# Kernel optimization log

Measured on AMD Instinct MI355X. Metric: run time of the kernel, lower is better.

Reference implementation:

```python
import jax, jax.numpy as jnp
import numpy as np

N = 8192
D_MODEL = 1024
KEY_DIM = 64
OUT_DIM = 1024
N_HEADS = 1
SCALE = N_HEADS ** (-0.5)  # = 1.0
NEG_INF = -1e10  # matches tf -10000000000.0


def setup_inputs() -> dict:
    key = jax.random.key(0)
    ks = jax.random.split(key, 3)
    x = jax.random.normal(ks[0], (N, D_MODEL), dtype=jnp.float32)
    w_qkv = jax.random.normal(ks[1], (D_MODEL, 3 * KEY_DIM), dtype=jnp.float32) * (D_MODEL ** -0.5)
    b_qkv = jnp.zeros((3 * KEY_DIM,), dtype=jnp.float32)
    w_out = jax.random.normal(ks[2], (KEY_DIM, OUT_DIM), dtype=jnp.float32) * (KEY_DIM ** -0.5)
    b_out = jnp.zeros((OUT_DIM,), dtype=jnp.float32)
    return {"x": x, "w_qkv": w_qkv, "b_qkv": b_qkv, "w_out": w_out, "b_out": b_out, "causal": 1}


def reference(x, w_qkv, b_qkv, w_out, b_out, causal):
    n = x.shape[-2]
    qkv = x @ w_qkv + b_qkv                      # [n, 3*key_dim]
    q, k, v = jnp.split(qkv, 3, axis=-1)         # each [n, key_dim]
    sim = jnp.einsum('id,jd->ij', q, k) * SCALE  # [n, n]
    if causal:
        mask = jnp.tril(jnp.ones((n, n), dtype=bool))
        sim = jnp.where(mask, sim, NEG_INF)
    attn = jax.nn.softmax(sim, axis=-1)          # [n, n]
    out = jnp.einsum('ij,jd->id', attn, v)       # [n, key_dim]
    return out @ w_out + b_out                   # [n, out_dim]
```

## Files before the change

### kernel.cpp

```cpp
#include <hip/hip_runtime.h>
#include <hip/hip_bf16.h>
#include <math.h>

#define N_TOK 8192
#define DM 1024
#define KD 64
#define ODIM 1024
#define LOG2E 1.4426950408889634f

typedef unsigned short ushort_t;
typedef __attribute__((ext_vector_type(8))) short short8;
typedef __attribute__((ext_vector_type(4))) float f32x4;

#define MFMA16(a, b, c) __builtin_amdgcn_mfma_f32_16x16x32_bf16((a), (b), (c), 0, 0, 0)

__device__ __forceinline__ float ex2(float x) {
#if __has_builtin(__builtin_amdgcn_exp2f)
    return __builtin_amdgcn_exp2f(x);
#else
    return exp2f(x);
#endif
}
__device__ __forceinline__ ushort_t rne(float x) {
    unsigned u = __float_as_uint(x);
    u += 0x7fffu + ((u >> 16) & 1u);
    return (ushort_t)(u >> 16);
}
__device__ __forceinline__ float ubf(ushort_t h) {
    return __uint_as_float(((unsigned)h) << 16);
}
__device__ __forceinline__ void split2(float x, ushort_t& hi, ushort_t& lo) {
    hi = rne(x);
    lo = rne(x - ubf(hi));
}
__device__ __forceinline__ unsigned bfpack(float a, float b) {
    unsigned ua = __float_as_uint(a); ua += 0x7fffu + ((ua >> 16) & 1u);
    unsigned ub = __float_as_uint(b); ub += 0x7fffu + ((ub >> 16) & 1u);
    return (ua >> 16) | (ub & 0xffff0000u);
}
__device__ __forceinline__ void gld_lds16(const void* g, void* l) {
    __builtin_amdgcn_global_load_lds(
        (const __attribute__((address_space(1))) unsigned int*)g,
        (__attribute__((address_space(3))) unsigned int*)l, 16, 0, 0);
}

__global__ __launch_bounds__(256) void prep_kernel(
    const float* __restrict__ wq, const float* __restrict__ wo,
    const float* __restrict__ x,
    ushort_t* __restrict__ wT_hi, ushort_t* __restrict__ wT_lo,
    ushort_t* __restrict__ woT_hi, ushort_t* __restrict__ woT_lo,
    ushort_t* __restrict__ x_hi, ushort_t* __restrict__ x_lo)
{
    const int idx = blockIdx.x * 256 + threadIdx.x;
    if (idx < 192 * 1024) {
        const int c = idx >> 10, k = idx & 1023;
        ushort_t h, l; split2(wq[k * 192 + c], h, l);
        wT_hi[idx] = h; wT_lo[idx] = l;
    } else if (idx < 256 * 1024) {
        const int j = idx - 192 * 1024;
        const int c = j >> 6, k = j & 63;
        ushort_t h, l; split2(wo[k * ODIM + c], h, l);
        woT_hi[j] = h; woT_lo[j] = l;
    } else {
        const size_t j = (size_t)(idx - 256 * 1024) * 8;
        const float4 xa = *(const float4*)&x[j];
        const float4 xb = *(const float4*)&x[j + 4];
        const float xe[8] = {xa.x, xa.y, xa.z, xa.w, xb.x, xb.y, xb.z, xb.w};
        union { short8 v; ushort_t u[8]; } hh, ll;
#pragma unroll
        for (int e = 0; e < 8; ++e) { split2(xe[e], hh.u[e], ll.u[e]); }
        *(short8*)&x_hi[j] = hh.v;
        *(short8*)&x_lo[j] = ll.v;
    }
}

__global__ __launch_bounds__(256) void qkv_kernel(
    const ushort_t* __restrict__ x_hi, const ushort_t* __restrict__ x_lo,
    const ushort_t* __restrict__ wT_hi, const ushort_t* __restrict__ wT_lo,
    const float* __restrict__ b,
    ushort_t* __restrict__ q_hi, ushort_t* __restrict__ q_lo,
    ushort_t* __restrict__ k_hi, ushort_t* __restrict__ k_lo,
    ushort_t* __restrict__ vT)
{
    __shared__ ushort_t S[2][20480];

    const int tid = threadIdx.x;
    const int wv = tid >> 6, lane = tid & 63, g = lane >> 4, i = lane & 15;
    const int bb = (int)blockIdx.x;
    const int R0 = (bb >> 1) * 64, h = bb & 1;
    const int rh = wv >> 1, cq = wv & 1;
    const int sub = lane >> 3, s = lane & 7;
    const f32x4 zero4 = {0.f, 0.f, 0.f, 0.f};

    auto stage = [&](int buf, int t) {
        const int kb = t * 64;
#pragma unroll
        for (int j = 0; j < 10; ++j) {
            const int c = wv + 4 * j;
            ushort_t* dst = &S[buf][c << 9];
            const ushort_t* src;
            if (j < 4) {
                const int r = ((c & 7) << 3) + sub;
                src = (j < 2 ? x_hi : x_lo) +
                      (size_t)(R0 + r) * DM + kb + ((s ^ (r & 7)) << 3);
            } else if (j < 7) {
                const int wc = ((c - 16) << 3) + sub;
                src = wT_hi + (size_t)(h * 96 + wc) * DM + kb + ((s ^ (wc & 7)) << 3);
            } else {
                const int wc = ((c - 28) << 3) + sub;
                src = wT_lo + (size_t)(h * 96 + wc) * DM + kb + ((s ^ (wc & 7)) << 3);
            }
            gld_lds16(src, dst);
        }
    };

    f32x4 acc[2][3] = {{zero4, zero4, zero4}, {zero4, zero4, zero4}};

    stage(0, 0);

    for (int t = 0; t < 16; ++t) {
        const int cur = t & 1;
        if (t + 1 < 16) {
            stage(cur ^ 1, t + 1);
            asm volatile("s_waitcnt vmcnt(10)" ::: "memory");
        } else {
            asm volatile("s_waitcnt vmcnt(0)" ::: "memory");
        }
        __builtin_amdgcn_s_barrier();

        const ushort_t* Sb = S[cur];
        short8 ah[2][2], al[2][2], bh[3][2], bl[3][2];
#pragma unroll
        for (int a = 0; a < 2; ++a) {
            const int r = (rh << 5) + (a << 4) + i;
#pragma unroll
            for (int kf = 0; kf < 2; ++kf) {
                const int off = (r << 6) + (((g + (kf << 2)) ^ (r & 7)) << 3);
                ah[a][kf] = *(const short8*)&Sb[off];
                al[a][kf] = *(const short8*)&Sb[4096 + off];
            }
        }
#pragma unroll
        for (int ct = 0; ct < 3; ++ct) {
            const int wc = cq * 48 + (ct << 4) + i;
#pragma unroll
            for (int kf = 0; kf < 2; ++kf) {
                const int off = (wc << 6) + (((g + (kf << 2)) ^ (wc & 7)) << 3);
                bh[ct][kf] = *(const short8*)&Sb[8192 + off];
                bl[ct][kf] = *(const short8*)&Sb[14336 + off];
            }
        }
#pragma unroll
        for (int a = 0; a < 2; ++a)
#pragma unroll
            for (int ct = 0; ct < 3; ++ct) {
                f32x4 v = acc[a][ct];
                v = MFMA16(ah[a][0], bh[ct][0], v);
                v = MFMA16(ah[a][1], bh[ct][1], v);
                v = MFMA16(ah[a][0], bl[ct][0], v);
                v = MFMA16(ah[a][1], bl[ct][1], v);
                v = MFMA16(al[a][0], bh[ct][0], v);
                v = MFMA16(al[a][1], bh[ct][1], v);
                acc[a][ct] = v;
            }
        asm volatile("s_waitcnt lgkmcnt(0)" ::: "memory");
        __builtin_amdgcn_s_barrier();
    }

#pragma unroll
    for (int ct = 0; ct < 3; ++ct) {
        const int ctid = h * 6 + cq * 3 + ct;
        const int col = (ctid << 4) + i;
        const float bias = b[col];
#pragma unroll
        for (int a = 0; a < 2; ++a) {
            const int row0 = R0 + (rh << 5) + (a << 4) + (g << 2);
            if (ctid < 4) {
#pragma unroll
                for (int reg = 0; reg < 4; ++reg) {
                    ushort_t hh, ll; split2((acc[a][ct][reg] + bias) * LOG2E, hh, ll);
                    q_hi[(row0 + reg) * KD + col] = hh;
                    q_lo[(row0 + reg) * KD + col] = ll;
                }
            } else if (ctid < 8) {
                const int c2 = col - 64;
#pragma unroll
                for (int reg = 0; reg < 4; ++reg) {
                    ushort_t hh, ll; split2(acc[a][ct][reg] + bias, hh, ll);
                    k_hi[(row0 + reg) * KD + c2] = hh;
                    k_lo[(row0 + reg) * KD + c2] = ll;
                }
            } else {
                union { ushort_t u[4]; uint2 v; } pk;
#pragma unroll
                for (int reg = 0; reg < 4; ++reg) pk.u[reg] = rne(acc[a][ct][reg] + bias);
                *(uint2*)&vT[(size_t)(col - 128) * N_TOK + row0] = pk.v;
            }
        }
    }
}

__global__ __launch_bounds__(256) void attn_kernel(
    const ushort_t* __restrict__ q_hi, const ushort_t* __restrict__ q_lo,
    const ushort_t* __restrict__ k_hi, const ushort_t* __restrict__ k_lo,
    const ushort_t* __restrict__ vT,
    float* __restrict__ Opart, float* __restrict__ MLpart,
    const int* __restrict__ causal_p, const int LC, const int ACT)
{
    __shared__ ushort_t Kls[2][2][4096];

    const int tid = threadIdx.x;
    const int wv = tid >> 6, lane = tid & 63, g = lane >> 4, i = lane & 15;
    const int causal = *causal_p;
    const f32x4 zero4 = {0.f, 0.f, 0.f, 0.f};
    const int ibase = ((i >> 2) << 3) + (i & 3);

    const int bb = (int)blockIdx.x;
    int gb, chunk;
    if (bb < ACT) {
        const int Q = 1 << (LC - 1);
        int a = (int)((sqrtf((float)bb / (float)Q + 0.25f) - 0.5f));
        while (a > 0 && a * (a + 1) * Q > bb) --a;
        while ((a + 1) * (a + 2) * Q <= bb) ++a;
        const int r = bb - a * (a + 1) * Q;
        const int b2 = r / (a + 1);
        chunk = r - b2 * (a + 1);
        gb = (a << LC) + b2;
    } else {
        const int j = bb - ACT;
        gb = j & 127; chunk = j >> 7;
        if (chunk <= (gb >> LC)) return;
    }
    const int nkt = causal ? gb + 1 : (N_TOK / 64);
    const int t0 = chunk << LC;
    if (t0 >= nkt) return;
    const int tmax = t0 + (1 << LC);
    const int t1 = tmax < nkt ? tmax : nkt;
    const int R0w = (gb << 6) + (wv << 4);

    const short8 qh0 = *(const short8*)&q_hi[(R0w + i) * KD + g * 8];
    const short8 qh1 = *(const short8*)&q_hi[(R0w + i) * KD + 32 + g * 8];
    const short8 ql0 = *(const short8*)&q_lo[(R0w + i) * KD + g * 8];
    const short8 ql1 = *(const short8*)&q_lo[(R0w + i) * KD + 32 + g * 8];

    const int srow = lane >> 3;
    const int sslot = lane & 7;
    auto stageK = [&](int nb, int t) {
        const int kb2 = t << 6;
#pragma unroll
        for (int h = 0; h < 2; ++h) {
            const int ch = wv + (h << 2);
            const int row = (ch << 3) + srow;
            const int sw = ((row & 3) << 1) | ((row >> 3) & 1);
            const size_t src = (size_t)(kb2 + row) * KD + ((sslot ^ sw) << 3);
            gld_lds16(&k_hi[src], &Kls[nb][0][ch << 9]);
            gld_lds16(&k_lo[src], &Kls[nb][1][ch << 9]);
        }
    };

    f32x4 o4[4] = {zero4, zero4, zero4, zero4};
    float runm = -1e30f, runl = 0.f;

    stageK(0, t0);

    for (int t = t0; t < t1; ++t) {
        const int cur = (t - t0) & 1;
        const int kb = t << 6;
        const bool more = (t + 1 < t1);

        short8 va0[4], va1[4];
#pragma unroll
        for (int ct2 = 0; ct2 < 4; ++ct2) {
            const size_t vrow = (size_t)(ct2 * 16 + i) * N_TOK + kb;
            va0[ct2] = *(const short8*)&vT[vrow + g * 8];
            va1[ct2] = *(const short8*)&vT[vrow + 32 + g * 8];
        }
        if (more) {
            stageK(cur ^ 1, t + 1);
            asm volatile("s_waitcnt vmcnt(12)" ::: "memory");
        } else {
            asm volatile("s_waitcnt vmcnt(8)" ::: "memory");
        }
        __builtin_amdgcn_s_barrier();

        f32x4 s4[4];
#pragma unroll
        for (int ct = 0; ct < 4; ++ct) {
            const int r = ((ct & 1) << 2) + ((ct >> 1) << 5) + ibase;
            const int sw = ((r & 3) << 1) | ((r >> 3) & 1);
            const ushort_t* khp = &Kls[cur][0][r << 6];
            const ushort_t* klp = &Kls[cur][1][r << 6];
            const short8 kh0 = *(const short8*)&khp[(g ^ sw) << 3];
            const short8 kh1 = *(const short8*)&khp[((g + 4) ^ sw) << 3];
            const short8 kl0 = *(const short8*)&klp[(g ^ sw) << 3];
            const short8 kl1 = *(const short8*)&klp[((g + 4) ^ sw) << 3];
            f32x4 a = MFMA16(kh0, qh0, zero4);
            a = MFMA16(kh1, qh1, a);
            a = MFMA16(kh0, ql0, a);
            a = MFMA16(kh1, ql1, a);
            a = MFMA16(kl0, qh0, a);
            a = MFMA16(kl1, qh1, a);
            s4[ct] = a;
        }
        asm volatile("s_waitcnt lgkmcnt(0)" ::: "memory");
        __builtin_amdgcn_s_barrier();

        if (causal && (kb + 64 > R0w)) {
#pragma unroll
            for (int ct = 0; ct < 4; ++ct) {
                const int kba = kb + ((ct & 1) << 2) + ((ct >> 1) << 5);
#pragma unroll
                for (int reg = 0; reg < 4; ++reg) {
                    const int key = kba + (g << 3) + reg;
                    s4[ct][reg] = (key <= R0w + i) ? s4[ct][reg] : -1e30f;
                }
            }
        }
        float mx = -1e30f;
#pragma unroll
        for (int ct = 0; ct < 4; ++ct)
#pragma unroll
            for (int reg = 0; reg < 4; ++reg) mx = fmaxf(mx, s4[ct][reg]);
        mx = fmaxf(mx, __shfl_xor(mx, 16));
        mx = fmaxf(mx, __shfl_xor(mx, 32));
        const bool defer = __all(mx - runm <= 8.0f);
        const float nm = defer ? runm : fmaxf(runm, mx);
        const float al = defer ? 1.0f : ex2(runm - nm);
        runm = nm;
        float rs = 0.f;
#pragma unroll
        for (int ct = 0; ct < 4; ++ct)
#pragma unroll
            for (int reg = 0; reg < 4; ++reg) {
                const float p = ex2(s4[ct][reg] - nm);
                s4[ct][reg] = p;
                rs += p;
            }
        rs += __shfl_xor(rs, 16);
        rs += __shfl_xor(rs, 32);
        runl = runl * al + rs;
        if (!defer) {
#pragma unroll
            for (int ct2 = 0; ct2 < 4; ++ct2)
#pragma unroll
                for (int reg = 0; reg < 4; ++reg) o4[ct2][reg] *= al;
        }
        short8 pb0, pb1;
        {
            union { unsigned w[4]; short8 v; } u;
            u.w[0] = bfpack(s4[0][0], s4[0][1]); u.w[1] = bfpack(s4[0][2], s4[0][3]);
            u.w[2] = bfpack(s4[1][0], s4[1][1]); u.w[3] = bfpack(s4[1][2], s4[1][3]);
            pb0 = u.v;
            u.w[0] = bfpack(s4[2][0], s4[2][1]); u.w[1] = bfpack(s4[2][2], s4[2][3]);
            u.w[2] = bfpack(s4[3][0], s4[3][1]); u.w[3] = bfpack(s4[3][2], s4[3][3]);
            pb1 = u.v;
        }
        if (more) asm volatile("s_waitcnt vmcnt(4)" ::: "memory");
        else      asm volatile("s_waitcnt vmcnt(0)" ::: "memory");
#pragma unroll
        for (int ct2 = 0; ct2 < 4; ++ct2) {
            o4[ct2] = MFMA16(va0[ct2], pb0, o4[ct2]);
            o4[ct2] = MFMA16(va1[ct2], pb1, o4[ct2]);
        }
    }

    const int pidx = ((gb << (7 - LC)) + chunk) * 4 + wv;
#pragma unroll
    for (int ct2 = 0; ct2 < 4; ++ct2)
#pragma unroll
        for (int reg = 0; reg < 4; ++reg) {
            const int d = ct2 * 16 + 4 * g + reg;
            Opart[((size_t)pidx * 16 + i) * 64 + d] = o4[ct2][reg];
        }
    if (lane < 16) {
        MLpart[pidx * 32 + lane] = runm;
        MLpart[pidx * 32 + 16 + lane] = runl;
    }
}

__global__ __launch_bounds__(256) void merge_kernel(
    const float* __restrict__ Opart, const float* __restrict__ MLpart,
    ushort_t* __restrict__ aoh, ushort_t* __restrict__ aol,
    const int* __restrict__ causal_p, const int LC)
{
    const int idx = blockIdx.x * 256 + threadIdx.x;
    const int d = idx & 63, row = idx >> 6;
    const int r = row & 15, qtile = row >> 4, gb = row >> 6;
    const int causal = *causal_p;
    const int nkt = causal ? gb + 1 : (N_TOK / 64);
    const int nch = (nkt + (1 << LC) - 1) >> LC;
    const int pb = ((gb << (7 - LC)) << 2) + (qtile & 3);
    float m[16], l[16];
#pragma unroll
    for (int c = 0; c < 16; ++c) {
        if (c < nch) {
            m[c] = MLpart[(pb + 4 * c) * 32 + r];
            l[c] = MLpart[(pb + 4 * c) * 32 + 16 + r];
        } else { m[c] = -1e30f; l[c] = 0.f; }
    }
    float M = m[0];
#pragma unroll
    for (int c = 1; c < 16; ++c) M = fmaxf(M, m[c]);
    float den = 0.f, O = 0.f;
#pragma unroll
    for (int c = 0; c < 16; ++c) {
        const float e = ex2(m[c] - M);
        den += l[c] * e;
        if (c < nch)
            O += Opart[((size_t)(pb + 4 * c) * 16 + r) * 64 + d] * e;
    }
    ushort_t h, lo2; split2(O / den, h, lo2);
    aoh[row * 64 + d] = h;
    aol[row * 64 + d] = lo2;
}

__global__ __launch_bounds__(256) void proj_kernel(
    const ushort_t* __restrict__ aoh, const ushort_t* __restrict__ aol,
    const ushort_t* __restrict__ woT_hi, const ushort_t* __restrict__ woT_lo,
    const float* __restrict__ bo, float* __restrict__ out)
{
    const int tid = threadIdx.x;
    const int wv = tid >> 6, lane = tid & 63, g = lane >> 4, i = lane & 15;
    const int bb = (int)blockIdx.x;
    const int qtile = bb >> 2, qa = bb & 3;
    const int R0 = qtile << 4;
    const f32x4 zero4 = {0.f, 0.f, 0.f, 0.f};
    const short8 ah0 = *(const short8*)&aoh[(R0 + i) * 64 + g * 8];
    const short8 ah1 = *(const short8*)&aoh[(R0 + i) * 64 + 32 + g * 8];
    const short8 al0 = *(const short8*)&aol[(R0 + i) * 64 + g * 8];
    const short8 al1 = *(const short8*)&aol[(R0 + i) * 64 + 32 + g * 8];
#pragma unroll
    for (int cc = 0; cc < 4; ++cc) {
        const int col = (qa << 8) + ((wv << 2) + cc) * 16 + i;
        const short8 bh0 = *(const short8*)&woT_hi[col * KD + g * 8];
        const short8 bh1 = *(const short8*)&woT_hi[col * KD + 32 + g * 8];
        const short8 bl0 = *(const short8*)&woT_lo[col * KD + g * 8];
        const short8 bl1 = *(const short8*)&woT_lo[col * KD + 32 + g * 8];
        f32x4 acc = MFMA16(ah0, bh0, zero4);
        acc = MFMA16(ah1, bh1, acc);
        acc = MFMA16(ah0, bl0, acc);
        acc = MFMA16(ah1, bl1, acc);
        acc = MFMA16(al0, bh0, acc);
        acc = MFMA16(al1, bh1, acc);
        const float bias = bo[col];
#pragma unroll
        for (int reg = 0; reg < 4; ++reg)
            out[(size_t)(R0 + 4 * g + reg) * ODIM + col] = acc[reg] + bias;
    }
}

extern "C" void kernel_launch(void* const* d_in, const int* in_sizes, int n_in,
                              void* d_out, int out_size, void* d_ws, size_t ws_size,
                              hipStream_t stream) {
    const float* x     = (const float*)d_in[0];
    const float* w_qkv = (const float*)d_in[1];
    const float* b_qkv = (const float*)d_in[2];
    const float* w_out = (const float*)d_in[3];
    const float* b_out = (const float*)d_in[4];
    const int* causal  = (const int*)d_in[5];
    float* out         = (float*)d_out;

    const int LC  = (ws_size >= ((size_t)39 << 20)) ? 3 : 4;
    const int NCH = 128 >> LC;
    const int NA  = 128 >> LC;
    const int ACT = (1 << LC) * NA * (NA + 1) / 2;
    const size_t opart_bytes = (size_t)128 * NCH * 4 * 16 * 64 * 4;

    char* ws = (char*)d_ws;
    ushort_t* wT_hi  = (ushort_t*)(ws);
    ushort_t* wT_lo  = (ushort_t*)(ws + 393216);
    ushort_t* woT_hi = (ushort_t*)(ws + 786432);
    ushort_t* woT_lo = (ushort_t*)(ws + 917504);
    ushort_t* q_hi   = (ushort_t*)(ws + (1u << 20));
    ushort_t* q_lo   = (ushort_t*)(ws + (2u << 20));
    ushort_t* k_hi   = (ushort_t*)(ws + (3u << 20));
    ushort_t* k_lo   = (ushort_t*)(ws + (4u << 20));
    ushort_t* vT     = (ushort_t*)(ws + (5u << 20));
    ushort_t* x_hi   = (ushort_t*)(ws + (6u << 20));
    ushort_t* x_lo   = (ushort_t*)(ws + (22u << 20));
    float*    Opart  = (float*)(ws + (6u << 20));
    float*    MLpart = (float*)(ws + (6u << 20) + opart_bytes);
    ushort_t* aoh    = (ushort_t*)(ws + (1u << 20));
    ushort_t* aol    = (ushort_t*)(ws + (2u << 20));

    prep_kernel<<<5120, 256, 0, stream>>>(w_qkv, w_out, x, wT_hi, wT_lo,
                                          woT_hi, woT_lo, x_hi, x_lo);
    qkv_kernel<<<256, 256, 0, stream>>>(x_hi, x_lo, wT_hi, wT_lo, b_qkv,
                                        q_hi, q_lo, k_hi, k_lo, vT);
    attn_kernel<<<ACT + NCH * 128, 256, 0, stream>>>(q_hi, q_lo, k_hi, k_lo, vT,
                                                     Opart, MLpart, causal, LC, ACT);
    merge_kernel<<<2048, 256, 0, stream>>>(Opart, MLpart, aoh, aol, causal, LC);
    proj_kernel<<<2048, 256, 0, stream>>>(aoh, aol, woT_hi, woT_lo, b_out, out);
}
```

Before: 194.1 us.

## Double attention block to 8 waves over 128 query rows sharing K tiles

Attention blocks now use 512 threads, with each of 8 waves handling 16 query rows, so one staged K tile in LDS serves 128 queries instead of 64. This halves global K traffic and LDS staging per query. Each wave now issues one K load pair instead of two, and the block grid is remapped over 128-row query groups. Waves whose rows lie entirely before the causal diagonal skip compute but still join the barriers. The cost is idle waves on diagonal tiles, and larger blocks may lower occupancy or scheduling flexibility.

Result: slower. 199.5 us (+2.8%).

```diff
diff --git a/kernel.cpp b/kernel.cpp
--- a/kernel.cpp
+++ b/kernel.cpp
@@ -200,7 +200,7 @@
     }
 }
 
-__global__ __launch_bounds__(256) void attn_kernel(
+__global__ __launch_bounds__(512) void attn_kernel(
     const ushort_t* __restrict__ q_hi, const ushort_t* __restrict__ q_lo,
     const ushort_t* __restrict__ k_hi, const ushort_t* __restrict__ k_lo,
     const ushort_t* __restrict__ vT,
@@ -216,27 +216,31 @@
     const int ibase = ((i >> 2) << 3) + (i & 3);
 
     const int bb = (int)blockIdx.x;
-    int gb, chunk;
+    const int G = 1 << (LC - 1);
+    int gb2, chunk;
     if (bb < ACT) {
-        const int Q = 1 << (LC - 1);
-        int a = (int)((sqrtf((float)bb / (float)Q + 0.25f) - 0.5f));
-        while (a > 0 && a * (a + 1) * Q > bb) --a;
-        while ((a + 1) * (a + 2) * Q <= bb) ++a;
-        const int r = bb - a * (a + 1) * Q;
+        int a = (int)(sqrtf((float)(2 * bb) / (float)G + 0.25f) - 0.5f);
+        while (a > 0 && G * a * (a + 1) / 2 > bb) --a;
+        while (G * (a + 1) * (a + 2) / 2 <= bb) ++a;
+        const int r = bb - G * a * (a + 1) / 2;
         const int b2 = r / (a + 1);
         chunk = r - b2 * (a + 1);
-        gb = (a << LC) + b2;
+        gb2 = G * a + b2;
     } else {
         const int j = bb - ACT;
-        gb = j & 127; chunk = j >> 7;
-        if (chunk <= (gb >> LC)) return;
-    }
-    const int nkt = causal ? gb + 1 : (N_TOK / 64);
+        gb2 = j & 63; chunk = j >> 6;
+        if (chunk <= (gb2 >> (LC - 1))) return;
+    }
+    const int nktB = causal ? 2 * gb2 + 2 : (N_TOK / 64);
     const int t0 = chunk << LC;
-    if (t0 >= nkt) return;
+    if (t0 >= nktB) return;
     const int tmax = t0 + (1 << LC);
-    const int t1 = tmax < nkt ? tmax : nkt;
-    const int R0w = (gb << 6) + (wv << 4);
+    const int t1 = tmax < nktB ? tmax : nktB;
+
+    const int qt = gb2 * 8 + wv;
+    const int R0w = qt << 4;
+    const int myNkt = causal ? (R0w >> 6) + 1 : (N_TOK / 64);
+    const int t1w = t1 < myNkt ? t1 : myNkt;
 
     const short8 qh0 = *(const short8*)&q_hi[(R0w + i) * KD + g * 8];
     const short8 qh1 = *(const short8*)&q_hi[(R0w + i) * KD + 32 + g * 8];
@@ -247,15 +251,11 @@
     const int sslot = lane & 7;
     auto stageK = [&](int nb, int t) {
         const int kb2 = t << 6;
-#pragma unroll
-        for (int h = 0; h < 2; ++h) {
-            const int ch = wv + (h << 2);
-            const int row = (ch << 3) + srow;
-            const int sw = ((row & 3) << 1) | ((row >> 3) & 1);
-            const size_t src = (size_t)(kb2 + row) * KD + ((sslot ^ sw) << 3);
-            gld_lds16(&k_hi[src], &Kls[nb][0][ch << 9]);
-            gld_lds16(&k_lo[src], &Kls[nb][1][ch << 9]);
-        }
+        const int row = (wv << 3) + srow;
+        const int sw = ((row & 3) << 1) | ((row >> 3) & 1);
+        const size_t src = (size_t)(kb2 + row) * KD + ((sslot ^ sw) << 3);
+        gld_lds16(&k_hi[src], &Kls[nb][0][wv << 9]);
+        gld_lds16(&k_lo[src], &Kls[nb][1][wv << 9]);
     };
 
     f32x4 o4[4] = {zero4, zero4, zero4, zero4};
@@ -267,104 +267,114 @@
         const int cur = (t - t0) & 1;
         const int kb = t << 6;
         const bool more = (t + 1 < t1);
+        const bool act = (t < t1w);
 
         short8 va0[4], va1[4];
-#pragma unroll
-        for (int ct2 = 0; ct2 < 4; ++ct2) {
-            const size_t vrow = (size_t)(ct2 * 16 + i) * N_TOK + kb;
-            va0[ct2] = *(const short8*)&vT[vrow + g * 8];
-            va1[ct2] = *(const short8*)&vT[vrow + 32 + g * 8];
+        if (act) {
+#pragma unroll
+            for (int ct2 = 0; ct2 < 4; ++ct2) {
+                const size_t vrow = (size_t)(ct2 * 16 + i) * N_TOK + kb;
+                va0[ct2] = *(const short8*)&vT[vrow + g * 8];
+                va1[ct2] = *(const short8*)&vT[vrow + 32 + g * 8];
+            }
         }
         if (more) {
             stageK(cur ^ 1, t + 1);
-            asm volatile("s_waitcnt vmcnt(12)" ::: "memory");
+            if (act) asm volatile("s_waitcnt vmcnt(10)" ::: "memory");
+            else     asm volatile("s_waitcnt vmcnt(2)" ::: "memory");
         } else {
-            asm volatile("s_waitcnt vmcnt(8)" ::: "memory");
+            if (act) asm volatile("s_waitcnt vmcnt(8)" ::: "memory");
+            else     asm volatile("s_waitcnt vmcnt(0)" ::: "memory");
         }
         __builtin_amdgcn_s_barrier();
 
-        f32x4 s4[4];
-#pragma unroll
-        for (int ct = 0; ct < 4; ++ct) {
-            const int r = ((ct & 1) << 2) + ((ct >> 1) << 5) + ibase;
-            const int sw = ((r & 3) << 1) | ((r >> 3) & 1);
-            const ushort_t* khp = &Kls[cur][0][r << 6];
-            const ushort_t* klp = &Kls[cur][1][r << 6];
-            const short8 kh0 = *(const short8*)&khp[(g ^ sw) << 3];
-            const short8 kh1 = *(const short8*)&khp[((g + 4) ^ sw) << 3];
-            const short8 kl0 = *(const short8*)&klp[(g ^ sw) << 3];
-            const short8 kl1 = *(const short8*)&klp[((g + 4) ^ sw) << 3];
-            f32x4 a = MFMA16(kh0, qh0, zero4);
-            a = MFMA16(kh1, qh1, a);
-            a = MFMA16(kh0, ql0, a);
-            a = MFMA16(kh1, ql1, a);
-            a = MFMA16(kl0, qh0, a);
-            a = MFMA16(kl1, qh1, a);
-            s4[ct] = a;
-        }
-        asm volatile("s_waitcnt lgkmcnt(0)" ::: "memory");
-        __builtin_amdgcn_s_barrier();
-
-        if (causal && (kb + 64 > R0w)) {
+        if (act) {
+            f32x4 s4[4];
 #pragma unroll
             for (int ct = 0; ct < 4; ++ct) {
-                const int kba = kb + ((ct & 1) << 2) + ((ct >> 1) << 5);
+                const int r = ((ct & 1) << 2) + ((ct >> 1) << 5) + ibase;
+                const int sw = ((r & 3) << 1) | ((r >> 3) & 1);
+                const ushort_t* khp = &Kls[cur][0][r << 6];
+                const ushort_t* klp = &Kls[cur][1][r << 6];
+                const short8 kh0 = *(const short8*)&khp[(g ^ sw) << 3];
+                const short8 kh1 = *(const short8*)&khp[((g + 4) ^ sw) << 3];
+                const short8 kl0 = *(const short8*)&klp[(g ^ sw) << 3];
+                const short8 kl1 = *(const short8*)&klp[((g + 4) ^ sw) << 3];
+                f32x4 a = MFMA16(kh0, qh0, zero4);
+                a = MFMA16(kh1, qh1, a);
+                a = MFMA16(kh0, ql0, a);
+                a = MFMA16(kh1, ql1, a);
+                a = MFMA16(kl0, qh0, a);
+                a = MFMA16(kl1, qh1, a);
+                s4[ct] = a;
+            }
+            asm volatile("s_waitcnt lgkmcnt(0)" ::: "memory");
+            __builtin_amdgcn_s_barrier();
+
+            if (causal && (kb + 64 > R0w)) {
+#pragma unroll
+                for (int ct = 0; ct < 4; ++ct) {
+                    const int kba = kb + ((ct & 1) << 2) + ((ct >> 1) << 5);
+#pragma unroll
+                    for (int reg = 0; reg < 4; ++reg) {
+                        const int key = kba + (g << 3) + reg;
+                        s4[ct][reg] = (key <= R0w + i) ? s4[ct][reg] : -1e30f;
+                    }
+                }
+            }
+            float mx = -1e30f;
+#pragma unroll
+            for (int ct = 0; ct < 4; ++ct)
+#pragma unroll
+                for (int reg = 0; reg < 4; ++reg) mx = fmaxf(mx, s4[ct][reg]);
+            mx = fmaxf(mx, __shfl_xor(mx, 16));
+            mx = fmaxf(mx, __shfl_xor(mx, 32));
+            const bool defer = __all(mx - runm <= 8.0f);
+            const float nm = defer ? runm : fmaxf(runm, mx);
+            const float al = defer ? 1.0f : ex2(runm - nm);
+            runm = nm;
+            float rs = 0.f;
+#pragma unroll
+            for (int ct = 0; ct < 4; ++ct)
 #pragma unroll
                 for (int reg = 0; reg < 4; ++reg) {
-                    const int key = kba + (g << 3) + reg;
-                    s4[ct][reg] = (key <= R0w + i) ? s4[ct][reg] : -1e30f;
+                    const float p = ex2(s4[ct][reg] - nm);
+                    s4[ct][reg] = p;
+                    rs += p;
                 }
-            }
-        }
-        float mx = -1e30f;
-#pragma unroll
-        for (int ct = 0; ct < 4; ++ct)
-#pragma unroll
-            for (int reg = 0; reg < 4; ++reg) mx = fmaxf(mx, s4[ct][reg]);
-        mx = fmaxf(mx, __shfl_xor(mx, 16));
-        mx = fmaxf(mx, __shfl_xor(mx, 32));
-        const bool defer = __all(mx - runm <= 8.0f);
-        const float nm = defer ? runm : fmaxf(runm, mx);
-        const float al = defer ? 1.0f : ex2(runm - nm);
-        runm = nm;
-        float rs = 0.f;
-#pragma unroll
-        for (int ct = 0; ct < 4; ++ct)
-#pragma unroll
-            for (int reg = 0; reg < 4; ++reg) {
-                const float p = ex2(s4[ct][reg] - nm);
-                s4[ct][reg] = p;
-                rs += p;
-            }
-        rs += __shfl_xor(rs, 16);
-        rs += __shfl_xor(rs, 32);
-        runl = runl * al + rs;
-        if (!defer) {
-#pragma unroll
-            for (int ct2 = 0; ct2 < 4; ++ct2)
-#pragma unroll
-                for (int reg = 0; reg < 4; ++reg) o4[ct2][reg] *= al;
-        }
-        short8 pb0, pb1;
-        {
-            union { unsigned w[4]; short8 v; } u;
-            u.w[0] = bfpack(s4[0][0], s4[0][1]); u.w[1] = bfpack(s4[0][2], s4[0][3]);
-            u.w[2] = bfpack(s4[1][0], s4[1][1]); u.w[3] = bfpack(s4[1][2], s4[1][3]);
-            pb0 = u.v;
-            u.w[0] = bfpack(s4[2][0], s4[2][1]); u.w[1] = bfpack(s4[2][2], s4[2][3]);
-            u.w[2] = bfpack(s4[3][0], s4[3][1]); u.w[3] = bfpack(s4[3][2], s4[3][3]);
-            pb1 = u.v;
-        }
-        if (more) asm volatile("s_waitcnt vmcnt(4)" ::: "memory");
-        else      asm volatile("s_waitcnt vmcnt(0)" ::: "memory");
-#pragma unroll
-        for (int ct2 = 0; ct2 < 4; ++ct2) {
-            o4[ct2] = MFMA16(va0[ct2], pb0, o4[ct2]);
-            o4[ct2] = MFMA16(va1[ct2], pb1, o4[ct2]);
-        }
-    }
-
-    const int pidx = ((gb << (7 - LC)) + chunk) * 4 + wv;
+            rs += __shfl_xor(rs, 16);
+            rs += __shfl_xor(rs, 32);
+            runl = runl * al + rs;
+            if (!defer) {
+#pragma unroll
+                for (int ct2 = 0; ct2 < 4; ++ct2)
+#pragma unroll
+                    for (int reg = 0; reg < 4; ++reg) o4[ct2][reg] *= al;
+            }
+            short8 pb0, pb1;
+            {
+                union { unsigned w[4]; short8 v; } u;
+                u.w[0] = bfpack(s4[0][0], s4[0][1]); u.w[1] = bfpack(s4[0][2], s4[0][3]);
+                u.w[2] = bfpack(s4[1][0], s4[1][1]); u.w[3] = bfpack(s4[1][2], s4[1][3]);
+                pb0 = u.v;
+                u.w[0] = bfpack(s4[2][0], s4[2][1]); u.w[1] = bfpack(s4[2][2], s4[2][3]);
+                u.w[2] = bfpack(s4[3][0], s4[3][1]); u.w[3] = bfpack(s4[3][2], s4[3][3]);
+                pb1 = u.v;
+            }
+            if (more) asm volatile("s_waitcnt vmcnt(2)" ::: "memory");
+            else      asm volatile("s_waitcnt vmcnt(0)" ::: "memory");
+#pragma unroll
+            for (int ct2 = 0; ct2 < 4; ++ct2) {
+                o4[ct2] = MFMA16(va0[ct2], pb0, o4[ct2]);
+                o4[ct2] = MFMA16(va1[ct2], pb1, o4[ct2]);
+            }
+        } else {
+            asm volatile("s_waitcnt lgkmcnt(0)" ::: "memory");
+            __builtin_amdgcn_s_barrier();
+        }
+    }
+
+    const int pidx = (((qt >> 2) << (7 - LC)) + chunk) * 4 + (qt & 3);
 #pragma unroll
     for (int ct2 = 0; ct2 < 4; ++ct2)
 #pragma unroll
@@ -462,8 +472,9 @@
 
     const int LC  = (ws_size >= ((size_t)39 << 20)) ? 3 : 4;
     const int NCH = 128 >> LC;
-    const int NA  = 128 >> LC;
-    const int ACT = (1 << LC) * NA * (NA + 1) / 2;
+    const int G   = 1 << (LC - 1);
+    const int NA2 = 64 / G;
+    const int ACT = G * NA2 * (NA2 + 1) / 2;
     const size_t opart_bytes = (size_t)128 * NCH * 4 * 16 * 64 * 4;
 
     char* ws = (char*)d_ws;
@@ -487,8 +498,8 @@
                                           woT_hi, woT_lo, x_hi, x_lo);
     qkv_kernel<<<256, 256, 0, stream>>>(x_hi, x_lo, wT_hi, wT_lo, b_qkv,
                                         q_hi, q_lo, k_hi, k_lo, vT);
-    attn_kernel<<<ACT + NCH * 128, 256, 0, stream>>>(q_hi, q_lo, k_hi, k_lo, vT,
-                                                     Opart, MLpart, causal, LC, ACT);
+    attn_kernel<<<ACT + 64 * (128 >> LC), 512, 0, stream>>>(
+        q_hi, q_lo, k_hi, k_lo, vT, Opart, MLpart, causal, LC, ACT);
     merge_kernel<<<2048, 256, 0, stream>>>(Opart, MLpart, aoh, aol, causal, LC);
     proj_kernel<<<2048, 256, 0, stream>>>(aoh, aol, woT_hi, woT_lo, b_out, out);
 }
```

## Stage V tiles through LDS with async loads alongside K, add MFMA priority

Applied to the files above, without the earlier changes.

The V tile is now copied into a third LDS plane with the same async global-to-LDS loads and XOR swizzle used for K, instead of each lane loading V straight from global memory into registers. The second barrier moves to the end of the iteration so the buffer is not overwritten while V is still being read. s_setprio brackets the two MFMA phases. This cuts redundant global V traffic and register pressure, at the cost of more LDS space and extra LDS reads per tile.

Result: faster. 174.5 us (-10.1%).

```diff
diff --git a/kernel.cpp b/kernel.cpp
--- a/kernel.cpp
+++ b/kernel.cpp
@@ -207,7 +207,7 @@
     float* __restrict__ Opart, float* __restrict__ MLpart,
     const int* __restrict__ causal_p, const int LC, const int ACT)
 {
-    __shared__ ushort_t Kls[2][2][4096];
+    __shared__ ushort_t Kls[2][3][4096];
 
     const int tid = threadIdx.x;
     const int wv = tid >> 6, lane = tid & 63, g = lane >> 4, i = lane & 15;
@@ -252,9 +252,11 @@
             const int ch = wv + (h << 2);
             const int row = (ch << 3) + srow;
             const int sw = ((row & 3) << 1) | ((row >> 3) & 1);
-            const size_t src = (size_t)(kb2 + row) * KD + ((sslot ^ sw) << 3);
-            gld_lds16(&k_hi[src], &Kls[nb][0][ch << 9]);
-            gld_lds16(&k_lo[src], &Kls[nb][1][ch << 9]);
+            const int slot = (sslot ^ sw) << 3;
+            const size_t ksrc = (size_t)(kb2 + row) * KD + slot;
+            gld_lds16(&k_hi[ksrc], &Kls[nb][0][ch << 9]);
+            gld_lds16(&k_lo[ksrc], &Kls[nb][1][ch << 9]);
+            gld_lds16(&vT[(size_t)row * N_TOK + kb2 + slot], &Kls[nb][2][ch << 9]);
         }
     };
 
@@ -268,22 +270,16 @@
         const int kb = t << 6;
         const bool more = (t + 1 < t1);
 
-        short8 va0[4], va1[4];
-#pragma unroll
-        for (int ct2 = 0; ct2 < 4; ++ct2) {
-            const size_t vrow = (size_t)(ct2 * 16 + i) * N_TOK + kb;
-            va0[ct2] = *(const short8*)&vT[vrow + g * 8];
-            va1[ct2] = *(const short8*)&vT[vrow + 32 + g * 8];
-        }
         if (more) {
             stageK(cur ^ 1, t + 1);
-            asm volatile("s_waitcnt vmcnt(12)" ::: "memory");
+            asm volatile("s_waitcnt vmcnt(6)" ::: "memory");
         } else {
-            asm volatile("s_waitcnt vmcnt(8)" ::: "memory");
+            asm volatile("s_waitcnt vmcnt(0)" ::: "memory");
         }
         __builtin_amdgcn_s_barrier();
 
         f32x4 s4[4];
+        __builtin_amdgcn_s_setprio(1);
 #pragma unroll
         for (int ct = 0; ct < 4; ++ct) {
             const int r = ((ct & 1) << 2) + ((ct >> 1) << 5) + ibase;
@@ -302,8 +298,7 @@
             a = MFMA16(kl1, qh1, a);
             s4[ct] = a;
         }
-        asm volatile("s_waitcnt lgkmcnt(0)" ::: "memory");
-        __builtin_amdgcn_s_barrier();
+        __builtin_amdgcn_s_setprio(0);
 
         if (causal && (kb + 64 > R0w)) {
 #pragma unroll
@@ -355,13 +350,20 @@
             u.w[2] = bfpack(s4[3][0], s4[3][1]); u.w[3] = bfpack(s4[3][2], s4[3][3]);
             pb1 = u.v;
         }
-        if (more) asm volatile("s_waitcnt vmcnt(4)" ::: "memory");
-        else      asm volatile("s_waitcnt vmcnt(0)" ::: "memory");
+        const ushort_t* Vb = &Kls[cur][2][0];
+        __builtin_amdgcn_s_setprio(1);
 #pragma unroll
         for (int ct2 = 0; ct2 < 4; ++ct2) {
-            o4[ct2] = MFMA16(va0[ct2], pb0, o4[ct2]);
-            o4[ct2] = MFMA16(va1[ct2], pb1, o4[ct2]);
-        }
+            const int r2 = ct2 * 16 + i;
+            const int sw2 = ((r2 & 3) << 1) | ((r2 >> 3) & 1);
+            const short8 va0 = *(const short8*)&Vb[(r2 << 6) + ((g ^ sw2) << 3)];
+            const short8 va1 = *(const short8*)&Vb[(r2 << 6) + (((g + 4) ^ sw2) << 3)];
+            o4[ct2] = MFMA16(va0, pb0, o4[ct2]);
+            o4[ct2] = MFMA16(va1, pb1, o4[ct2]);
+        }
+        __builtin_amdgcn_s_setprio(0);
+        asm volatile("s_waitcnt lgkmcnt(0)" ::: "memory");
+        __builtin_amdgcn_s_barrier();
     }
 
     const int pidx = ((gb << (7 - LC)) + chunk) * 4 + wv;
```
